# Kernel tuning notes

Hardware: AMD Instinct MI355X
Metric: run time of the kernel (lower is better)

## Reference

```python
import jax, jax.numpy as jnp
import numpy as np

B, T, I, H, O = 128, 1024, 128, 1024, 128

def setup_inputs() -> dict:
    key = jax.random.key(0)
    ks = jax.random.split(key, 11)
    s = 1.0 / np.sqrt(H)  # torch default LSTM init scale
    return {
        "x": jax.random.normal(ks[0], (B, T, I), jnp.float32),
        "sequence_length": jax.random.randint(ks[1], (B,), 0, T, jnp.int64 if jax.config.jax_enable_x64 else jnp.int32),
        "hn": jax.random.normal(ks[2], (B, H), jnp.float32),
        "cn": jax.random.normal(ks[3], (B, H), jnp.float32),
        "output_t": jax.random.normal(ks[4], (B, O), jnp.float32),
        "W_ih": jax.random.normal(ks[5], (4 * H, I + O), jnp.float32) * s,
        "W_hh": jax.random.normal(ks[6], (4 * H, H), jnp.float32) * s,
        "b_ih": jax.random.normal(ks[7], (4 * H,), jnp.float32) * s,
        "b_hh": jax.random.normal(ks[8], (4 * H,), jnp.float32) * s,
        "W_out": jax.random.normal(ks[9], (O, H), jnp.float32) * s,
        "b_out": jax.random.normal(ks[10], (O,), jnp.float32) * s,
    }

def reference(x, sequence_length, hn, cn, output_t, W_ih, W_hh, b_ih, b_hh, W_out, b_out):
    # eval mode (self.training=False): no dropout applied
    Tn = x.shape[1]
    Hd = hn.shape[-1]
    # masks[t, b] = 1.0 if sequence_length[b] > t
    masks = (jnp.arange(Tn)[:, None] < sequence_length[None, :]).astype(x.dtype)  # [T, B]
    xs = jnp.transpose(x, (1, 0, 2))  # [T, B, I]
    bias = b_ih + b_hh

    def step(carry, inp):
        h, c, out_t = carry
        xt, m = inp                      # xt [B,I], m [B]
        m = m[:, None]                   # [B,1]
        lstm_in = jnp.concatenate([xt * m, out_t], axis=-1)  # [B, I+O]
        gates = lstm_in @ W_ih.T + h @ W_hh.T + bias          # [B, 4H]
        i_g, f_g, g_g, o_g = jnp.split(gates, 4, axis=-1)     # torch gate order i,f,g,o
        i_g = jax.nn.sigmoid(i_g)
        f_g = jax.nn.sigmoid(f_g)
        g_g = jnp.tanh(g_g)
        o_g = jax.nn.sigmoid(o_g)
        c = f_g * c + i_g * g_g
        h = o_g * jnp.tanh(c)
        out_t = h @ W_out.T + b_out      # [B, O]
        return (h, c, out_t), out_t * m

    (_, _, _), ys = jax.lax.scan(step, (hn, cn, output_t), (xs, masks))
    return jnp.transpose(ys, (1, 0, 2))  # [B, T, O]
```

## Files before the change

kernel.cpp:

```cpp
#include <hip/hip_runtime.h>
#include <stdint.h>

#define Tn 1024
#define In 128

typedef __attribute__((ext_vector_type(8))) short short8;
typedef __attribute__((ext_vector_type(4))) float f32x4;
typedef unsigned long long u64;

#define WS_WFRAG  0ull
#define WS_WOUT   (WS_WFRAG + 10485760ull)
#define WS_Z0     (WS_WOUT + 262144ull)
#define WS_HBUF   (WS_Z0 + 32768ull)
#define WS_BIAS   (WS_HBUF + 524288ull)
#define WS_CNT    (WS_BIAS + 16384ull)

__device__ __forceinline__ unsigned short f2bf(float f) {
  unsigned u = __builtin_bit_cast(unsigned, f);
  return (unsigned short)((u + 0x7FFFu + ((u >> 16) & 1u)) >> 16);
}
__device__ __forceinline__ float fast_sig(float v) {
  float e = __builtin_amdgcn_exp2f(-1.44269504089f * v);
  return __builtin_amdgcn_rcpf(1.0f + e);
}
__device__ __forceinline__ float fast_tanh(float v) {
  float a = fabsf(v);
  float e = __builtin_amdgcn_exp2f(-2.88539008178f * a);
  float r = (1.0f - e) * __builtin_amdgcn_rcpf(1.0f + e);
  return copysignf(r, v);
}

__global__ void k_wfrag(const float* __restrict__ Wih, const float* __restrict__ Whh,
                        const float* __restrict__ Wout, char* __restrict__ ws) {
  const int u = blockIdx.x, nt = blockIdx.y, kt = blockIdx.z;
  const int lane = threadIdx.x;
  const int col = lane & 15, quad = lane >> 4;
  const int r = nt * 16 + col;
  const int g = r >> 5, jj = r & 31;
  const int n = g * 1024 + u * 32 + jj;
  float v[8];
  if (kt < 32) {
    const int k = kt * 32 + quad * 8;
    #pragma unroll
    for (int e = 0; e < 8; e++) v[e] = Whh[(size_t)n * 1024 + k + e];
    const float* wo = Wih + (size_t)n * 256 + 128;
    for (int o = 0; o < 128; o++) {
      const float wv = wo[o];
      const float* wr = Wout + (size_t)o * 1024 + k;
      #pragma unroll
      for (int e = 0; e < 8; e++) v[e] = fmaf(wv, wr[e], v[e]);
    }
  } else if (kt < 36) {
    const int k = (kt - 32) * 32 + quad * 8;
    #pragma unroll
    for (int e = 0; e < 8; e++) v[e] = Wih[(size_t)n * 256 + k + e];
  } else {
    const int o = (kt - 36) * 32 + quad * 8;
    #pragma unroll
    for (int e = 0; e < 8; e++) v[e] = Wih[(size_t)n * 256 + 128 + o + e];
  }
  short8 pk;
  #pragma unroll
  for (int e = 0; e < 8; e++) pk[e] = (short)f2bf(v[e]);
  *(short8*)(ws + WS_WFRAG + ((size_t)((u * 8 + nt) * 40 + kt) * 64 + lane) * 16) = pk;
}

__global__ void k_misc(const float* __restrict__ Wout, const float* __restrict__ hn,
                       const float* __restrict__ out_t, const float* __restrict__ bout,
                       const float* __restrict__ bih, const float* __restrict__ bhh,
                       const float* __restrict__ Wih, float* __restrict__ outp,
                       char* __restrict__ ws) {
  const int blk = blockIdx.x, lane = threadIdx.x;
  const int col = lane & 15, quad = lane >> 4;
  if (blk < 256) {
    const int u = blk >> 5, kt = blk & 31;
    const int o = u * 16 + col, j0 = kt * 32 + quad * 8;
    short8 pk;
    #pragma unroll
    for (int e = 0; e < 8; e++) pk[e] = (short)f2bf(Wout[(size_t)o * 1024 + j0 + e]);
    *(short8*)(ws + WS_WOUT + ((size_t)(u * 32 + kt) * 64 + lane) * 16) = pk;
  } else if (blk < 512) {
    const int t2 = blk - 256;
    const int mm = t2 >> 5, kt = t2 & 31;
    const int b = mm * 16 + col, j0 = kt * 32 + quad * 8;
    short8 pk;
    #pragma unroll
    for (int e = 0; e < 8; e++) pk[e] = (short)f2bf(hn[(size_t)b * 1024 + j0 + e]);
    *(short8*)(ws + WS_HBUF + ((size_t)((8 + mm) * 32 + kt) * 64 + lane) * 16) = pk;
  } else if (blk < 544) {
    const int t2 = blk - 512;
    const int mm = t2 >> 2, kz = t2 & 3;
    const int b = mm * 16 + col;
    const int o0 = kz * 32 + quad * 8;
    float acc[8];
    #pragma unroll
    for (int e = 0; e < 8; e++) acc[e] = out_t[(size_t)b * 128 + o0 + e] - bout[o0 + e];
    for (int j = 0; j < 1024; j += 4) {
      const f32x4 h4 = *(const f32x4*)(hn + (size_t)b * 1024 + j);
      #pragma unroll
      for (int e = 0; e < 8; e++) {
        const f32x4 w4 = *(const f32x4*)(Wout + (size_t)(o0 + e) * 1024 + j);
        acc[e] -= h4[0] * w4[0] + h4[1] * w4[1] + h4[2] * w4[2] + h4[3] * w4[3];
      }
    }
    short8 pk;
    #pragma unroll
    for (int e = 0; e < 8; e++) pk[e] = (short)f2bf(acc[e]);
    *(short8*)(ws + WS_Z0 + ((size_t)(mm * 4 + kz) * 64 + lane) * 16) = pk;
  } else if (blk < 608) {
    const int n = (blk - 544) * 64 + lane;
    float v = bih[n] + bhh[n];
    const float* wo = Wih + (size_t)n * 256 + 128;
    for (int o = 0; o < 128; o++) v = fmaf(wo[o], bout[o], v);
    ((float*)(ws + WS_BIAS))[n] = v;
  } else if (blk < 616) {
    int* c = (int*)(ws + WS_CNT);
    const int base = ((blk - 608) * 64 + lane) * 16;
    #pragma unroll
    for (int k = 0; k < 16; k++) c[base + k] = 0;
  } else {
    int* c = (int*)outp;
    #pragma unroll
    for (int k = 0; k < 8; k++) c[lane * 8 + k] = 0;
  }
}

__launch_bounds__(512, 2)
__global__ void k_main(const float* __restrict__ x, const int* __restrict__ seq,
                       const float* __restrict__ cn, const float* __restrict__ b_out,
                       float* __restrict__ out, char* __restrict__ ws) {
  __shared__ short8 a_lds[40 * 64];
  __shared__ float  gates_lds[128 * 20];
  __shared__ short8 htile[64];
  __shared__ float  ysred[8 * 16 * 20];
  __shared__ float  bias_lds[128];
  __shared__ float  bo_lds[16];
  __shared__ int    seq_lds[16];

  const int tid  = threadIdx.x;
  const int lane = tid & 63;
  const int w    = tid >> 6;
  const int wg   = blockIdx.x;

  int* cnt = (int*)(ws + WS_CNT);

  int m_, u_, fast_;
  {
    int* ids = (int*)ysred;
    int* scr = (int*)out;
    if (tid == 0) {
      int myxcd;
      asm volatile("s_getreg_b32 %0, hwreg(HW_REG_XCC_ID)" : "=s"(myxcd));
      myxcd &= 7;
      ids[259] = myxcd;
      __hip_atomic_store(&scr[8 + wg], myxcd, __ATOMIC_RELAXED, __HIP_MEMORY_SCOPE_SYSTEM);
      __hip_atomic_fetch_add(&scr[0], 1, __ATOMIC_ACQ_REL, __HIP_MEMORY_SCOPE_SYSTEM);
      while (__hip_atomic_load(&scr[0], __ATOMIC_ACQUIRE, __HIP_MEMORY_SCOPE_SYSTEM) < 256) {}
    }
    __syncthreads();
    if (tid < 256)
      ids[tid] = __hip_atomic_load(&scr[8 + tid], __ATOMIC_RELAXED,
                                   __HIP_MEMORY_SCOPE_SYSTEM) & 7;
    __syncthreads();
    if (tid == 0) {
      const int myxcd = ids[259];
      int cx[8] = {0, 0, 0, 0, 0, 0, 0, 0};
      int rank = 0;
      for (int i = 0; i < 256; i++) {
        const int xi = ids[i];
        cx[xi]++;
        if (xi == myxcd && i < wg) rank++;
      }
      bool bal = true;
      for (int k = 0; k < 8; k++) bal = bal && (cx[k] == 32);
      ids[256] = bal ? myxcd : (wg & 7);
      ids[257] = bal ? rank : (wg >> 3);
      ids[258] = bal ? 1 : 0;
      __hip_atomic_fetch_add(&scr[1], 1, __ATOMIC_ACQ_REL, __HIP_MEMORY_SCOPE_SYSTEM);
      while (__hip_atomic_load(&scr[1], __ATOMIC_ACQUIRE, __HIP_MEMORY_SCOPE_SYSTEM) < 256) {}
    }
    __syncthreads();
    m_ = ids[256]; u_ = ids[257]; fast_ = ids[258];
    __syncthreads();
  }
  const int  m     = m_;
  const int  u     = u_;
  const bool fastp = (fast_ != 0);

  const char* wfrag = ws + WS_WFRAG;
  const char* woutf = ws + WS_WOUT;
  char* hbuf  = ws + WS_HBUF;
  const float* bias2 = (const float*)(ws + WS_BIAS);

  short8 bfr[40];
  {
    const char* base = wfrag + ((size_t)(u * 8 + w) * 40 * 64) * 16 + (size_t)lane * 16;
    #pragma unroll
    for (int kt = 0; kt < 40; kt++) bfr[kt] = *(const short8*)(base + (size_t)kt * 1024);
  }
  if (tid < 16) seq_lds[tid] = seq[m * 16 + tid];
  if (tid < 16 && u < 8) bo_lds[tid] = b_out[u * 16 + tid];
  if (tid < 128) {
    const int g = tid >> 5, jj = tid & 31;
    bias_lds[tid] = bias2[g * 1024 + u * 32 + jj];
  }
  const int b_loc  = tid & 15;
  const int jj_loc = tid >> 4;
  float c_reg = cn[(size_t)(m * 16 + b_loc) * 1024 + u * 32 + jj_loc];
  __syncthreads();

  #pragma unroll 1
  for (int tt = 0; tt <= Tn; tt++) {
    if (tt < Tn && tid < 256) {
      const int kt4 = tid >> 6, ln = tid & 63;
      const int b = ln & 15, quad = ln >> 4;
      const int i0 = kt4 * 32 + quad * 8;
      const float* xp = x + ((size_t)(m * 16 + b) * Tn + tt) * In + i0;
      const float mk = (tt < seq_lds[b]) ? 1.0f : 0.0f;
      const f32x4 x0 = *(const f32x4*)xp;
      const f32x4 x1 = *(const f32x4*)(xp + 4);
      short8 pk;
      pk[0] = (short)f2bf(x0[0] * mk); pk[1] = (short)f2bf(x0[1] * mk);
      pk[2] = (short)f2bf(x0[2] * mk); pk[3] = (short)f2bf(x0[3] * mk);
      pk[4] = (short)f2bf(x1[0] * mk); pk[5] = (short)f2bf(x1[1] * mk);
      pk[6] = (short)f2bf(x1[2] * mk); pk[7] = (short)f2bf(x1[3] * mk);
      a_lds[(32 + kt4) * 64 + ln] = pk;
    }
    if (tt == 0 && tid < 256) {
      const int kz = tid >> 6, ln = tid & 63;
      a_lds[(36 + kz) * 64 + ln] =
          *(const short8*)(ws + WS_Z0 + ((size_t)(m * 4 + kz) * 64 + ln) * 16);
    }
    if (tt >= 1 && tid == 0) {
      while (__hip_atomic_load(&cnt[m * 1024 + (tt - 1)], __ATOMIC_RELAXED,
                               __HIP_MEMORY_SCOPE_SYSTEM) < 32) {}
    }
    __syncthreads();
    {
      const char* srcb = hbuf + (size_t)((((tt + 1) & 1) * 8) + m) * 32768;
      if (fastp && tt >= 1) {
        const f32x4* sp = (const f32x4*)srcb;
        f32x4 t0, t1, t2, t3;
        asm volatile(
            "global_load_dwordx4 %0, %4, off sc0\n\t"
            "global_load_dwordx4 %1, %5, off sc0\n\t"
            "global_load_dwordx4 %2, %6, off sc0\n\t"
            "global_load_dwordx4 %3, %7, off sc0\n\t"
            "s_waitcnt vmcnt(0)"
            : "=&v"(t0), "=&v"(t1), "=&v"(t2), "=&v"(t3)
            : "v"(sp + tid), "v"(sp + 512 + tid), "v"(sp + 1024 + tid),
              "v"(sp + 1536 + tid)
            : "memory");
        f32x4* dst = (f32x4*)a_lds;
        dst[tid] = t0; dst[512 + tid] = t1; dst[1024 + tid] = t2; dst[1536 + tid] = t3;
      } else {
        const u64* src = (const u64*)srcb;
        u64 tmp[8];
        #pragma unroll
        for (int s = 0; s < 8; s++)
          tmp[s] = __hip_atomic_load(&src[s * 512 + tid], __ATOMIC_RELAXED,
                                     __HIP_MEMORY_SCOPE_SYSTEM);
        u64* dst = (u64*)a_lds;
        #pragma unroll
        for (int s = 0; s < 8; s++) dst[s * 512 + tid] = tmp[s];
      }
    }
    __syncthreads();

    if (tt < Tn) {
      const float bias_v = bias_lds[w * 16 + (lane & 15)];
      f32x4 acc0 = {bias_v, bias_v, bias_v, bias_v};
      f32x4 acc1 = {0.f, 0.f, 0.f, 0.f};
      #pragma unroll
      for (int kt = 0; kt < 36; kt += 2) {
        const short8 a0 = a_lds[kt * 64 + lane];
        const short8 a1 = a_lds[(kt + 1) * 64 + lane];
        acc0 = __builtin_amdgcn_mfma_f32_16x16x32_bf16(a0, bfr[kt], acc0, 0, 0, 0);
        acc1 = __builtin_amdgcn_mfma_f32_16x16x32_bf16(a1, bfr[kt + 1], acc1, 0, 0, 0);
      }
      if (tt == 0) {
        #pragma unroll
        for (int kt = 36; kt < 40; kt += 2) {
          const short8 a0 = a_lds[kt * 64 + lane];
          const short8 a1 = a_lds[(kt + 1) * 64 + lane];
          acc0 = __builtin_amdgcn_mfma_f32_16x16x32_bf16(a0, bfr[kt], acc0, 0, 0, 0);
          acc1 = __builtin_amdgcn_mfma_f32_16x16x32_bf16(a1, bfr[kt + 1], acc1, 0, 0, 0);
        }
      }
      {
        const int r = w * 16 + (lane & 15);
        const int bq = (lane >> 4) * 4;
        f32x4 s;
        s[0] = acc0[0] + acc1[0]; s[1] = acc0[1] + acc1[1];
        s[2] = acc0[2] + acc1[2]; s[3] = acc0[3] + acc1[3];
        *(f32x4*)&gates_lds[r * 20 + bq] = s;
      }
      __syncthreads();
      {
        const float Gi = gates_lds[(0 * 32 + jj_loc) * 20 + b_loc];
        const float Gf = gates_lds[(1 * 32 + jj_loc) * 20 + b_loc];
        const float Gg = gates_lds[(2 * 32 + jj_loc) * 20 + b_loc];
        const float Go = gates_lds[(3 * 32 + jj_loc) * 20 + b_loc];
        const float ig = fast_sig(Gi), fg = fast_sig(Gf);
        const float gg = fast_tanh(Gg), og = fast_sig(Go);
        c_reg = fg * c_reg + ig * gg;
        const float h = og * fast_tanh(c_reg);
        ((short*)htile)[(b_loc + 16 * (jj_loc >> 3)) * 8 + (jj_loc & 7)] = (short)f2bf(h);
      }
      __syncthreads();
      if (tid < 64) {
        const short8 v = htile[lane];
        char* dstb = hbuf + (size_t)((tt & 1) * 8 + m) * 32768 + (size_t)u * 1024 +
                     (size_t)lane * 16;
        if (fastp) {
          asm volatile("global_store_dwordx4 %0, %1, off sc0" :: "v"(dstb), "v"(v)
                       : "memory");
        } else {
          u64* dstp = (u64*)dstb;
          const u64* pv = (const u64*)&v;
          __hip_atomic_store(&dstp[0], pv[0], __ATOMIC_RELAXED, __HIP_MEMORY_SCOPE_SYSTEM);
          __hip_atomic_store(&dstp[1], pv[1], __ATOMIC_RELAXED, __HIP_MEMORY_SCOPE_SYSTEM);
        }
        asm volatile("s_waitcnt vmcnt(0)" ::: "memory");
        if (tid == 0)
          __hip_atomic_fetch_add(&cnt[m * 1024 + tt], 1, __ATOMIC_RELAXED,
                                 __HIP_MEMORY_SCOPE_SYSTEM);
      }
    }

    if (u < 8 && tt >= 1) {
      f32x4 yacc = {0.f, 0.f, 0.f, 0.f};
      const char* wob = woutf + ((size_t)(u * 32 + w * 4) * 64 + lane) * 16;
      #pragma unroll
      for (int i = 0; i < 4; i++) {
        const short8 bf = *(const short8*)(wob + (size_t)i * 1024);
        const short8 af = a_lds[(w * 4 + i) * 64 + lane];
        yacc = __builtin_amdgcn_mfma_f32_16x16x32_bf16(af, bf, yacc, 0, 0, 0);
      }
      {
        const int o = lane & 15, bq = (lane >> 4) * 4;
        *(f32x4*)&ysred[(w * 16 + o) * 20 + bq] = yacc;
      }
      __syncthreads();
      if (tid < 256) {
        const int o = tid & 15, b = tid >> 4;
        float s = 0.f;
        #pragma unroll
        for (int q = 0; q < 8; q++) s += ysred[(q * 16 + o) * 20 + b];
        s += bo_lds[o];
        const float val = ((tt - 1) < seq_lds[b]) ? s : 0.0f;
        out[((size_t)(m * 16 + b) * Tn + (tt - 1)) * 128 + u * 16 + o] = val;
      }
    }
  }
}

extern "C" void kernel_launch(void* const* d_in, const int* in_sizes, int n_in,
                              void* d_out, int out_size, void* d_ws, size_t ws_size,
                              hipStream_t stream) {
  (void)in_sizes; (void)n_in; (void)out_size; (void)ws_size;
  const float* x    = (const float*)d_in[0];
  const int*   seq  = (const int*)d_in[1];
  const float* hn   = (const float*)d_in[2];
  const float* cn   = (const float*)d_in[3];
  const float* outt = (const float*)d_in[4];
  const float* Wih  = (const float*)d_in[5];
  const float* Whh  = (const float*)d_in[6];
  const float* bih  = (const float*)d_in[7];
  const float* bhh  = (const float*)d_in[8];
  const float* Wout = (const float*)d_in[9];
  const float* bout = (const float*)d_in[10];
  float* out = (float*)d_out;
  char* ws = (char*)d_ws;

  hipLaunchKernelGGL(k_wfrag, dim3(32, 8, 40), dim3(64), 0, stream, Wih, Whh, Wout, ws);
  hipLaunchKernelGGL(k_misc, dim3(617), dim3(64), 0, stream, Wout, hn, outt, bout,
                     bih, bhh, Wih, out, ws);
  void* args[] = {(void*)&x, (void*)&seq, (void*)&cn, (void*)&bout, (void*)&out, (void*)&ws};
  hipLaunchCooperativeKernel((const void*)k_main, dim3(256), dim3(512), args, 0, stream);
}
```

Before: 3.216 ms.

## Interleave gate rows in weight fragments so each lane holds all four gates

The packed weight layout now interleaves the i,f,g,o gate rows, and the MFMA operands are swapped so each lane's accumulator holds the four gates of one hidden unit for one batch row. This removes the gates LDS buffer, its store/reload and one block-wide barrier per timestep. The bias is kept in registers, and four independent accumulators replace two to give the matrix unit more instruction-level parallelism. A barrier is added at the end of the output stage to protect buffer reuse, which puts back some of the synchronisation cost.

```diff
diff --git a/kernel.cpp b/kernel.cpp
--- a/kernel.cpp
+++ b/kernel.cpp
@@ -35,9 +35,7 @@
   const int u = blockIdx.x, nt = blockIdx.y, kt = blockIdx.z;
   const int lane = threadIdx.x;
   const int col = lane & 15, quad = lane >> 4;
-  const int r = nt * 16 + col;
-  const int g = r >> 5, jj = r & 31;
-  const int n = g * 1024 + u * 32 + jj;
+  const int n = (col & 3) * 1024 + u * 32 + nt * 4 + (col >> 2);
   float v[8];
   if (kt < 32) {
     const int k = kt * 32 + quad * 8;
@@ -130,10 +128,8 @@
                        const float* __restrict__ cn, const float* __restrict__ b_out,
                        float* __restrict__ out, char* __restrict__ ws) {
   __shared__ short8 a_lds[40 * 64];
-  __shared__ float  gates_lds[128 * 20];
   __shared__ short8 htile[64];
   __shared__ float  ysred[8 * 16 * 20];
-  __shared__ float  bias_lds[128];
   __shared__ float  bo_lds[16];
   __shared__ int    seq_lds[16];
 
@@ -200,21 +196,22 @@
   }
   if (tid < 16) seq_lds[tid] = seq[m * 16 + tid];
   if (tid < 16 && u < 8) bo_lds[tid] = b_out[u * 16 + tid];
-  if (tid < 128) {
-    const int g = tid >> 5, jj = tid & 31;
-    bias_lds[tid] = bias2[g * 1024 + u * 32 + jj];
-  }
-  const int b_loc  = tid & 15;
-  const int jj_loc = tid >> 4;
-  float c_reg = cn[(size_t)(m * 16 + b_loc) * 1024 + u * 32 + jj_loc];
+
+  const int col16 = lane & 15;
+  const int quad  = lane >> 4;
+  const int jj_my = w * 4 + quad;
+  float bias_g[4];
+  #pragma unroll
+  for (int j = 0; j < 4; j++) bias_g[j] = bias2[j * 1024 + u * 32 + jj_my];
+  float c_reg = cn[(size_t)(m * 16 + col16) * 1024 + u * 32 + jj_my];
   __syncthreads();
 
   #pragma unroll 1
   for (int tt = 0; tt <= Tn; tt++) {
     if (tt < Tn && tid < 256) {
       const int kt4 = tid >> 6, ln = tid & 63;
-      const int b = ln & 15, quad = ln >> 4;
-      const int i0 = kt4 * 32 + quad * 8;
+      const int b = ln & 15, qd = ln >> 4;
+      const int i0 = kt4 * 32 + qd * 8;
       const float* xp = x + ((size_t)(m * 16 + b) * Tn + tt) * In + i0;
       const float mk = (tt < seq_lds[b]) ? 1.0f : 0.0f;
       const f32x4 x0 = *(const f32x4*)xp;
@@ -268,44 +265,41 @@
     __syncthreads();
 
     if (tt < Tn) {
-      const float bias_v = bias_lds[w * 16 + (lane & 15)];
-      f32x4 acc0 = {bias_v, bias_v, bias_v, bias_v};
+      f32x4 acc0 = {bias_g[0], bias_g[1], bias_g[2], bias_g[3]};
       f32x4 acc1 = {0.f, 0.f, 0.f, 0.f};
+      f32x4 acc2 = {0.f, 0.f, 0.f, 0.f};
+      f32x4 acc3 = {0.f, 0.f, 0.f, 0.f};
       #pragma unroll
-      for (int kt = 0; kt < 36; kt += 2) {
-        const short8 a0 = a_lds[kt * 64 + lane];
-        const short8 a1 = a_lds[(kt + 1) * 64 + lane];
-        acc0 = __builtin_amdgcn_mfma_f32_16x16x32_bf16(a0, bfr[kt], acc0, 0, 0, 0);
-        acc1 = __builtin_amdgcn_mfma_f32_16x16x32_bf16(a1, bfr[kt + 1], acc1, 0, 0, 0);
+      for (int kk = 0; kk < 9; kk++) {
+        const short8 a0 = a_lds[(kk * 4 + 0) * 64 + lane];
+        const short8 a1 = a_lds[(kk * 4 + 1) * 64 + lane];
+        const short8 a2 = a_lds[(kk * 4 + 2) * 64 + lane];
+        const short8 a3 = a_lds[(kk * 4 + 3) * 64 + lane];
+        acc0 = __builtin_amdgcn_mfma_f32_16x16x32_bf16(bfr[kk * 4 + 0], a0, acc0, 0, 0, 0);
+        acc1 = __builtin_amdgcn_mfma_f32_16x16x32_bf16(bfr[kk * 4 + 1], a1, acc1, 0, 0, 0);
+        acc2 = __builtin_amdgcn_mfma_f32_16x16x32_bf16(bfr[kk * 4 + 2], a2, acc2, 0, 0, 0);
+        acc3 = __builtin_amdgcn_mfma_f32_16x16x32_bf16(bfr[kk * 4 + 3], a3, acc3, 0, 0, 0);
       }
       if (tt == 0) {
-        #pragma unroll
-        for (int kt = 36; kt < 40; kt += 2) {
-          const short8 a0 = a_lds[kt * 64 + lane];
-          const short8 a1 = a_lds[(kt + 1) * 64 + lane];
-          acc0 = __builtin_amdgcn_mfma_f32_16x16x32_bf16(a0, bfr[kt], acc0, 0, 0, 0);
-          acc1 = __builtin_amdgcn_mfma_f32_16x16x32_bf16(a1, bfr[kt + 1], acc1, 0, 0, 0);
-        }
+        const short8 z0 = a_lds[36 * 64 + lane];
+        const short8 z1 = a_lds[37 * 64 + lane];
+        const short8 z2 = a_lds[38 * 64 + lane];
+        const short8 z3 = a_lds[39 * 64 + lane];
+        acc0 = __builtin_amdgcn_mfma_f32_16x16x32_bf16(bfr[36], z0, acc0, 0, 0, 0);
+        acc1 = __builtin_amdgcn_mfma_f32_16x16x32_bf16(bfr[37], z1, acc1, 0, 0, 0);
+        acc2 = __builtin_amdgcn_mfma_f32_16x16x32_bf16(bfr[38], z2, acc2, 0, 0, 0);
+        acc3 = __builtin_amdgcn_mfma_f32_16x16x32_bf16(bfr[39], z3, acc3, 0, 0, 0);
       }
       {
-        const int r = w * 16 + (lane & 15);
-        const int bq = (lane >> 4) * 4;
-        f32x4 s;
-        s[0] = acc0[0] + acc1[0]; s[1] = acc0[1] + acc1[1];
-        s[2] = acc0[2] + acc1[2]; s[3] = acc0[3] + acc1[3];
-        *(f32x4*)&gates_lds[r * 20 + bq] = s;
-      }
-      __syncthreads();
-      {
-        const float Gi = gates_lds[(0 * 32 + jj_loc) * 20 + b_loc];
-        const float Gf = gates_lds[(1 * 32 + jj_loc) * 20 + b_loc];
-        const float Gg = gates_lds[(2 * 32 + jj_loc) * 20 + b_loc];
-        const float Go = gates_lds[(3 * 32 + jj_loc) * 20 + b_loc];
+        const float Gi = acc0[0] + acc1[0] + acc2[0] + acc3[0];
+        const float Gf = acc0[1] + acc1[1] + acc2[1] + acc3[1];
+        const float Gg = acc0[2] + acc1[2] + acc2[2] + acc3[2];
+        const float Go = acc0[3] + acc1[3] + acc2[3] + acc3[3];
         const float ig = fast_sig(Gi), fg = fast_sig(Gf);
         const float gg = fast_tanh(Gg), og = fast_sig(Go);
         c_reg = fg * c_reg + ig * gg;
         const float h = og * fast_tanh(c_reg);
-        ((short*)htile)[(b_loc + 16 * (jj_loc >> 3)) * 8 + (jj_loc & 7)] = (short)f2bf(h);
+        ((short*)htile)[(col16 + 16 * (jj_my >> 3)) * 8 + (jj_my & 7)] = (short)f2bf(h);
       }
       __syncthreads();
       if (tid < 64) {
@@ -351,6 +345,7 @@
         const float val = ((tt - 1) < seq_lds[b]) ? s : 0.0f;
         out[((size_t)(m * 16 + b) * Tn + (tt - 1)) * 128 + u * 16 + o] = val;
       }
+      __syncthreads();
     }
   }
 }
```

New measurement: 3.088 ms. 1.04x faster.
